# Kernel tuning notes

Hardware: AMD Instinct MI355X
Metric: run time of the kernel (lower is better)

The kernel has to match this reference:

```python
import jax, jax.numpy as jnp
import numpy as np

H = 12        # attention heads
WIN = 256     # one-sided sliding window (attention_window = 512)
L = 2         # encoder layers in this reference (full model: 12, same structure)
NEG = -1e9


def layer_norm(x, g, b, eps=1e-5):
    m = jnp.mean(x, axis=-1, keepdims=True)
    v = jnp.mean((x - m) ** 2, axis=-1, keepdims=True)
    return (x - m) * jax.lax.rsqrt(v + eps) * g + b


def heads(x):
    B, S, D = x.shape
    return x.reshape(B, S, H, D // H).transpose(0, 2, 1, 3)  # [B,H,S,Dh]


def overlap_chunks(x, w):
    # x: [B,H,S,D] -> [B,H,C,3w,D]; chunk c = keys/values seen by queries [c*w,(c+1)*w)
    B, Hh, S, D = x.shape
    xp = jnp.pad(x, ((0, 0), (0, 0), (w, w), (0, 0))).reshape(B, Hh, S // w + 2, w, D)
    return jnp.concatenate([xp[:, :, :-2], xp[:, :, 1:-1], xp[:, :, 2:]], axis=3)


def encoder_layer(x, mask, p):
    (Wq, bq, Wk, bk, Wv, bv, Wqg, bqg, Wkg, bkg, Wvg, bvg,
     Wo, bo, g1, b1n, W1, bf1, W2, bf2, g2, b2n) = p
    B, S, D = x.shape
    Dh = D // H
    w = WIN
    C = S // w
    scale = 1.0 / np.sqrt(Dh)
    q = heads(x @ Wq + bq)
    k = heads(x @ Wk + bk)
    v = heads(x @ Wv + bv)
    # --- sliding-window (banded) attention, chunked: each query chunk sees 3 key chunks ---
    qc = q.reshape(B, H, C, w, Dh)
    k3 = overlap_chunks(k, w)
    v3 = overlap_chunks(v, w)
    scores = jnp.einsum('bhcqd,bhckd->bhcqk', qc, k3) * scale  # [B,H,C,w,3w]
    qi = jnp.arange(w)[:, None]
    kr = jnp.arange(3 * w)[None, :] - w                       # key offset rel. to chunk start
    band = jnp.abs(kr - qi) <= w                              # [w,3w] |rel pos| <= w
    kpos = jnp.arange(C)[:, None] * w + (jnp.arange(3 * w) - w)[None, :]  # [C,3w] abs key idx
    inrange = (kpos >= 0) & (kpos < S)
    mp = jnp.pad(mask, ((0, 0), (w, w))).reshape(B, C + 2, w)
    m3 = jnp.concatenate([mp[:, :-2], mp[:, 1:-1], mp[:, 2:]], axis=2)  # [B,C,3w]
    loc_mask = band[None, :, :] & inrange[:, None, :]         # [C,w,3w]
    valid = loc_mask[None, None] & (m3 > 0)[:, None, :, None, :]
    scores = jnp.where(valid, scores, NEG)
    sloc = scores.reshape(B, H, S, 3 * w)
    # every token also attends to the global token (position 0)
    gsc = jnp.einsum('bhsd,bhd->bhs', q, k[:, :, 0]) * scale  # [B,H,S]
    attn = jax.nn.softmax(jnp.concatenate([sloc, gsc[..., None]], axis=-1), axis=-1)
    aloc = attn[..., :3 * w].reshape(B, H, C, w, 3 * w)
    ag = attn[..., -1]                                        # [B,H,S]
    out = jnp.einsum('bhcqk,bhckd->bhcqd', aloc, v3).reshape(B, H, S, Dh)
    out = out + ag[..., None] * v[:, :, 0][:, :, None, :]
    # --- global token full attention with separate global projections ---
    qg = heads(x @ Wqg + bqg)[:, :, 0]                        # [B,H,Dh]
    kg = heads(x @ Wkg + bkg)
    vg = heads(x @ Wvg + bvg)
    gs = jnp.where(mask[:, None, :] > 0,
                   jnp.einsum('bhd,bhsd->bhs', qg, kg) * scale, NEG)
    og = jnp.einsum('bhs,bhsd->bhd', jax.nn.softmax(gs, axis=-1), vg)
    out = out.at[:, :, 0].set(og)
    h = out.transpose(0, 2, 1, 3).reshape(B, S, D) @ Wo + bo
    x = layer_norm(x + h, g1, b1n)
    f = jax.nn.gelu(x @ W1 + bf1) @ W2 + bf2
    return layer_norm(x + f, g2, b2n)


def forward(input_ids, attention_mask, word_emb, pos_emb, ln_e_g, ln_e_b,
            Wq, bq, Wk, bk, Wv, bv, Wqg, bqg, Wkg, bkg, Wvg, bvg, Wo, bo,
            ln1_g, ln1_b, W1, bf1, W2, bf2, ln2_g, ln2_b, Wp, bp, Wc, bc):
    B, S = input_ids.shape
    x = word_emb[input_ids] + pos_emb[:S][None]
    x = layer_norm(x, ln_e_g, ln_e_b)
    for l in range(L):
        p = (Wq[l], bq[l], Wk[l], bk[l], Wv[l], bv[l], Wqg[l], bqg[l],
             Wkg[l], bkg[l], Wvg[l], bvg[l], Wo[l], bo[l], ln1_g[l], ln1_b[l],
             W1[l], bf1[l], W2[l], bf2[l], ln2_g[l], ln2_b[l])
        x = encoder_layer(x, attention_mask, p)
    pooled = jnp.tanh(x[:, 0] @ Wp + bp)   # BERT-style pooler on CLS
    return pooled @ Wc + bc


def setup_inputs() -> dict:
    B, S, D, V, F, NL = 2, 4096, 768, 50265, 3072, 2
    keys = iter(jax.random.split(jax.random.key(0), 64))
    def w(shape, s=0.02):
        return (jax.random.normal(next(keys), shape, jnp.float32) * s)
    inp = {
        'input_ids': jax.random.randint(next(keys), (B, S), 0, V),
        'attention_mask': jnp.ones((B, S), jnp.int32),
        'word_emb': w((V, D)), 'pos_emb': w((S, D)),
        'ln_e_g': jnp.ones((D,), jnp.float32), 'ln_e_b': jnp.zeros((D,), jnp.float32),
        'Wq': w((L, D, D)), 'bq': jnp.zeros((L, D), jnp.float32),
        'Wk': w((L, D, D)), 'bk': jnp.zeros((L, D), jnp.float32),
        'Wv': w((L, D, D)), 'bv': jnp.zeros((L, D), jnp.float32),
        'Wqg': w((L, D, D)), 'bqg': jnp.zeros((L, D), jnp.float32),
        'Wkg': w((L, D, D)), 'bkg': jnp.zeros((L, D), jnp.float32),
        'Wvg': w((L, D, D)), 'bvg': jnp.zeros((L, D), jnp.float32),
        'Wo': w((L, D, D)), 'bo': jnp.zeros((L, D), jnp.float32),
        'ln1_g': jnp.ones((L, D), jnp.float32), 'ln1_b': jnp.zeros((L, D), jnp.float32),
        'W1': w((L, D, F)), 'bf1': jnp.zeros((L, F), jnp.float32),
        'W2': w((L, F, D)), 'bf2': jnp.zeros((L, D), jnp.float32),
        'ln2_g': jnp.ones((L, D), jnp.float32), 'ln2_b': jnp.zeros((L, D), jnp.float32),
        'Wp': w((D, D)), 'bp': jnp.zeros((D,), jnp.float32),
        'Wc': w((D, NL)), 'bc': jnp.zeros((NL,), jnp.float32),
    }
    return inp


def reference(input_ids, attention_mask, word_emb, pos_emb, ln_e_g, ln_e_b,
              Wq, bq, Wk, bk, Wv, bv, Wqg, bqg, Wkg, bkg, Wvg, bvg, Wo, bo,
              ln1_g, ln1_b, W1, bf1, W2, bf2, ln2_g, ln2_b, Wp, bp, Wc, bc):
    return forward(input_ids, attention_mask, word_emb, pos_emb, ln_e_g, ln_e_b,
                   Wq, bq, Wk, bk, Wv, bv, Wqg, bqg, Wkg, bkg, Wvg, bvg, Wo, bo,
                   ln1_g, ln1_b, W1, bf1, W2, bf2, ln2_g, ln2_b, Wp, bp, Wc, bc)
```

## Files before the change

### kernel.cpp

```cpp
#include <hip/hip_runtime.h>
#include <hip/hip_bf16.h>
#include <math.h>

#define BB 2
#define SS 4096
#define DD 768
#define HH 12
#define DHH 64
#define WW 256
#define CC 16
#define FF 3072

typedef __attribute__((ext_vector_type(8))) short bf16x8;
typedef __attribute__((ext_vector_type(4))) float f32x4;

struct TP12 { const float* s[12]; unsigned short* d[12]; };
struct TP4  { const float* s[4];  unsigned short* d[4];  };

__device__ __forceinline__ float gelu_f(float x) {
    float u = 0.7978845608028654f * fmaf(0.044715f * x * x, x, x);
    return x / (1.f + __expf(-2.f * u));
}

__device__ __forceinline__ unsigned short bfb(float f) {
    __hip_bfloat16 h = __float2bfloat16(f);
    return *(unsigned short*)&h;
}

__device__ __forceinline__ float bf2f(unsigned short u) {
    return __uint_as_float(((unsigned int)u) << 16);
}

__device__ __forceinline__ void gload16(const void* g, void* l) {
    __builtin_amdgcn_global_load_lds(
        (const __attribute__((address_space(1))) unsigned int*)g,
        (__attribute__((address_space(3))) unsigned int*)l, 16, 0, 0);
}

__global__ __launch_bounds__(256) void transpose12_k(TP12 p)
{
    __shared__ float t[32][33];
    int z = blockIdx.z;
    const float* Wsrc = p.s[z];
    unsigned short* Wt = p.d[z];
    const int K = DD, N = DD;
    int n0 = blockIdx.x * 32, k0 = blockIdx.y * 32;
    int tx = threadIdx.x & 31, ty = threadIdx.x >> 5;
#pragma unroll
    for (int i = 0; i < 32; i += 8)
        t[ty + i][tx] = Wsrc[(size_t)(k0 + ty + i) * N + n0 + tx];
    __syncthreads();
#pragma unroll
    for (int i = 0; i < 32; i += 8)
        Wt[(size_t)(n0 + ty + i) * K + k0 + tx] = bfb(t[tx][ty + i]);
}

__global__ __launch_bounds__(256) void transposeR4_k(TP4 p)
{
    __shared__ float t[32][33];
    int z = blockIdx.z;
    const float* Wsrc = p.s[z];
    unsigned short* Wt = p.d[z];
    int K, N, n0, k0;
    if (z < 2) { K = DD; N = FF; n0 = blockIdx.x * 32; k0 = blockIdx.y * 32; }
    else { K = FF; N = DD; int cell = blockIdx.y * 96 + blockIdx.x;
           n0 = (cell % 24) * 32; k0 = (cell / 24) * 32; }
    int tx = threadIdx.x & 31, ty = threadIdx.x >> 5;
#pragma unroll
    for (int i = 0; i < 32; i += 8)
        t[ty + i][tx] = Wsrc[(size_t)(k0 + ty + i) * N + n0 + tx];
    __syncthreads();
#pragma unroll
    for (int i = 0; i < 32; i += 8)
        Wt[(size_t)(n0 + ty + i) * K + k0 + tx] = bfb(t[tx][ty + i]);
}

__global__ __launch_bounds__(256) void pack_bias5_k(const float* __restrict__ b0,
        const float* __restrict__ b1, const float* __restrict__ b2,
        const float* __restrict__ b3, const float* __restrict__ b4,
        float* __restrict__ dst)
{
    int gid = blockIdx.x * 256 + threadIdx.x;
    if (gid >= 2 * 5 * DD) return;
    int l = gid / (5 * DD), r = gid % (5 * DD), seg = r / DD, i = r % DD;
    const float* srcs[5] = { b0, b1, b2, b3, b4 };
    dst[gid] = srcs[seg][l * DD + i];
}

__global__ __launch_bounds__(256) void embed_ln_k(const int* __restrict__ ids,
        const float* __restrict__ wemb, const float* __restrict__ pemb,
        const float* __restrict__ g, const float* __restrict__ bta,
        float* __restrict__ x, unsigned short* __restrict__ xbf)
{
    int row = blockIdx.x;
    int s = row & (SS - 1);
    int tid = threadIdx.x;
    int lane = tid & 63, wvi = tid >> 6;
    __shared__ float red[8];
    float4 v = { 0.f, 0.f, 0.f, 0.f };
    if (tid < 192) {
        const float4* we = (const float4*)(wemb + (size_t)ids[row] * DD);
        const float4* pe = (const float4*)(pemb + (size_t)s * DD);
        float4 a = we[tid], b = pe[tid];
        v.x = a.x + b.x; v.y = a.y + b.y; v.z = a.z + b.z; v.w = a.w + b.w;
    }
    float sum = (v.x + v.y) + (v.z + v.w);
    float sq = fmaf(v.x, v.x, fmaf(v.y, v.y, fmaf(v.z, v.z, v.w * v.w)));
#pragma unroll
    for (int o = 1; o < 64; o <<= 1) {
        sum += __shfl_xor(sum, o);
        sq  += __shfl_xor(sq, o);
    }
    if (lane == 0) { red[wvi] = sum; red[4 + wvi] = sq; }
    __syncthreads();
    float S = (red[0] + red[1]) + (red[2] + red[3]);
    float Q = (red[4] + red[5]) + (red[6] + red[7]);
    float mean = S * (1.f / DD);
    float var = Q * (1.f / DD) - mean * mean;
    float rstd = rsqrtf(var + 1e-5f);
    if (tid < 192) {
        float4 gg = ((const float4*)g)[tid];
        float4 bb = ((const float4*)bta)[tid];
        float4 o;
        o.x = (v.x - mean) * rstd * gg.x + bb.x;
        o.y = (v.y - mean) * rstd * gg.y + bb.y;
        o.z = (v.z - mean) * rstd * gg.z + bb.z;
        o.w = (v.w - mean) * rstd * gg.w + bb.w;
        ((float4*)(x + (size_t)row * DD))[tid] = o;
        ushort4 ob = { bfb(o.x), bfb(o.y), bfb(o.z), bfb(o.w) };
        ((ushort4*)(xbf + (size_t)row * DD))[tid] = ob;
    }
}

__global__ __launch_bounds__(256) void add_ln_k(const float* __restrict__ xin,
        const float* __restrict__ hin, const float* __restrict__ g,
        const float* __restrict__ bta, float* __restrict__ xout,
        unsigned short* __restrict__ xbf)
{
    int row = blockIdx.x;
    int tid = threadIdx.x;
    int lane = tid & 63, wvi = tid >> 6;
    __shared__ float red[8];
    float4 v = { 0.f, 0.f, 0.f, 0.f };
    if (tid < 192) {
        float4 a = ((const float4*)(xin + (size_t)row * DD))[tid];
        float4 b = ((const float4*)(hin + (size_t)row * DD))[tid];
        v.x = a.x + b.x; v.y = a.y + b.y; v.z = a.z + b.z; v.w = a.w + b.w;
    }
    float sum = (v.x + v.y) + (v.z + v.w);
    float sq = fmaf(v.x, v.x, fmaf(v.y, v.y, fmaf(v.z, v.z, v.w * v.w)));
#pragma unroll
    for (int o = 1; o < 64; o <<= 1) {
        sum += __shfl_xor(sum, o);
        sq  += __shfl_xor(sq, o);
    }
    if (lane == 0) { red[wvi] = sum; red[4 + wvi] = sq; }
    __syncthreads();
    float S = (red[0] + red[1]) + (red[2] + red[3]);
    float Q = (red[4] + red[5]) + (red[6] + red[7]);
    float mean = S * (1.f / DD);
    float var = Q * (1.f / DD) - mean * mean;
    float rstd = rsqrtf(var + 1e-5f);
    if (tid < 192) {
        float4 gg = ((const float4*)g)[tid];
        float4 bb = ((const float4*)bta)[tid];
        float4 o;
        o.x = (v.x - mean) * rstd * gg.x + bb.x;
        o.y = (v.y - mean) * rstd * gg.y + bb.y;
        o.z = (v.z - mean) * rstd * gg.z + bb.z;
        o.w = (v.w - mean) * rstd * gg.w + bb.w;
        ((float4*)(xout + (size_t)row * DD))[tid] = o;
        ushort4 ob = { bfb(o.x), bfb(o.y), bfb(o.z), bfb(o.w) };
        ((ushort4*)(xbf + (size_t)row * DD))[tid] = ob;
    }
}

template<int OUT_BF16, int ACT_GELU>
__global__ __launch_bounds__(256) void mfma_gemm_k(
        const unsigned short* __restrict__ A,
        const unsigned short* __restrict__ Bt,
        const float* __restrict__ bias,
        void* __restrict__ Cv, int M, int N, int K)
{
    __shared__ short As[128 * 64];
    __shared__ short Bs[128 * 64];
    const int tid = threadIdx.x;
    const int lane = tid & 63, wv = tid >> 6;
    int nbx = gridDim.x;
    int nby = gridDim.y;
    int nwg = nbx * nby;
    int lid = blockIdx.y * nbx + blockIdx.x;
    int nid = ((nwg & 7) == 0) ? ((lid & 7) * (nwg >> 3) + (lid >> 3)) : lid;
    const int bm = (nid / nby) * 128, bn = (nid % nby) * 128;
    const int wm = wv >> 1, wn = wv & 1;

    const int srow0 = (tid * 16) >> 7;
    const int sbc   = (tid * 16) & 127;
    const int srcc  = sbc ^ ((srow0 & 7) << 4);
    const int ldst  = tid * 16;
    const char* Ab = (const char*)(A + (size_t)bm * K);
    const char* Bb = (const char*)(Bt + (size_t)bn * K);

    f32x4 acc[4][4];
#pragma unroll
    for (int i = 0; i < 4; i++)
#pragma unroll
        for (int j = 0; j < 4; j++) acc[i][j] = (f32x4){0.f, 0.f, 0.f, 0.f};

    const int lr = lane & 15;
    const int g = lane >> 4;
    const int rswz = (lr & 7) << 4;

    for (int k0 = 0; k0 < K; k0 += 64) {
        __syncthreads();
#pragma unroll
        for (int p = 0; p < 4; p++) {
            size_t roff = (size_t)(srow0 + p * 32) * (K * 2) + (size_t)k0 * 2 + srcc;
            gload16(Ab + roff, (char*)As + p * 4096 + ldst);
            gload16(Bb + roff, (char*)Bs + p * 4096 + ldst);
        }
        __syncthreads();
#pragma unroll
        for (int kk = 0; kk < 2; kk++) {
            int colb = (kk * 64 + g * 16) ^ rswz;
            bf16x8 af[4], bfr[4];
#pragma unroll
            for (int i = 0; i < 4; i++)
                af[i] = *(const bf16x8*)((const char*)As + (wm * 64 + i * 16 + lr) * 128 + colb);
#pragma unroll
            for (int j = 0; j < 4; j++)
                bfr[j] = *(const bf16x8*)((const char*)Bs + (wn * 64 + j * 16 + lr) * 128 + colb);
#pragma unroll
            for (int i = 0; i < 4; i++)
#pragma unroll
                for (int j = 0; j < 4; j++)
                    acc[i][j] = __builtin_amdgcn_mfma_f32_16x16x32_bf16(af[i], bfr[j], acc[i][j], 0, 0, 0);
        }
    }

    const int rq = lane >> 4;
#pragma unroll
    for (int j = 0; j < 4; j++) {
        int col = bn + wn * 64 + j * 16 + lr;
        float bv = bias[col];
#pragma unroll
        for (int i = 0; i < 4; i++) {
            int rowb = bm + wm * 64 + i * 16 + rq * 4;
#pragma unroll
            for (int r = 0; r < 4; r++) {
                float o = acc[i][j][r] + bv;
                if (ACT_GELU) o = gelu_f(o);
                if (OUT_BF16)
                    ((unsigned short*)Cv)[(size_t)(rowb + r) * N + col] = bfb(o);
                else
                    ((float*)Cv)[(size_t)(rowb + r) * N + col] = o;
            }
        }
    }
}

__global__ __launch_bounds__(256) void vtrans_k(const unsigned short* __restrict__ packed,
        unsigned short* __restrict__ vt)
{
    int s0 = blockIdx.x * 64, h = blockIdx.y, b = blockIdx.z;
    int tid = threadIdx.x;
    __shared__ unsigned short t[64][72];
    int r = tid >> 3, dc = (tid & 7) * 8;
#pragma unroll
    for (int half = 0; half < 2; half++) {
        int rr = r + half * 32;
        const unsigned short* src = packed + (size_t)(b * SS + s0 + rr) * 3840 + 2 * DD + h * 64 + dc;
        *(uint4*)&t[rr][dc] = *(const uint4*)src;
    }
    __syncthreads();
    int d = tid >> 3, sc = (tid & 7) * 8;
#pragma unroll
    for (int half = 0; half < 2; half++) {
        int dd2 = d + half * 32;
        unsigned short v[8];
#pragma unroll
        for (int e = 0; e < 8; e++) v[e] = t[sc + e][dd2];
        unsigned short* dst = vt + (size_t)((b * HH + h) * 64 + dd2) * SS + s0 + sc;
        *(uint4*)dst = *(uint4*)v;
    }
}

__global__ __launch_bounds__(256) void swin_mfma_k(
        const unsigned short* __restrict__ packed,
        const unsigned short* __restrict__ vt,
        const int* __restrict__ mask,
        unsigned short* __restrict__ O)
{
    __shared__ __align__(16) char smem[52736];
    const int c2 = blockIdx.x, h = blockIdx.y, b = blockIdx.z;
    const int tid = threadIdx.x;
    const int lane = tid & 63, wv = tid >> 6;
    const int l15 = lane & 15, g = lane >> 4;
    const int bh = b * HH + h;
    const int q0 = c2 * 128;

    char* PB = smem + 32768 + wv * 4096;
    float* maskAll = (float*)(smem + 49152);
    float* sA = (float*)(smem + 51712);
    float* sB = (float*)(smem + 52224);

    const char* pk_bytes = (const char*)packed;
    const char* vt_bytes = (const char*)vt;

    bf16x8 qf[2][2];
#pragma unroll
    for (int j = 0; j < 2; j++)
#pragma unroll
        for (int kk = 0; kk < 2; kk++)
            qf[j][kk] = *(const bf16x8*)(packed +
                (size_t)(b * SS + q0 + wv * 32 + j * 16 + l15) * 3840 + h * 64 + kk * 32 + g * 8);
    bf16x8 gkf[2];
#pragma unroll
    for (int kk = 0; kk < 2; kk++)
        gkf[kk] = *(const bf16x8*)(packed + (size_t)(b * SS) * 3840 + DD + h * 64 + kk * 32 + g * 8);
    float v0r[4];
#pragma unroll
    for (int jd = 0; jd < 4; jd++)
        v0r[jd] = bf2f(vt[(size_t)(bh * 64 + jd * 16 + l15) * SS]);

    f32x4 o_[2][4];
#pragma unroll
    for (int i = 0; i < 2; i++)
#pragma unroll
        for (int j = 0; j < 4; j++) o_[i][j] = (f32x4){0.f, 0.f, 0.f, 0.f};
    float m_[2] = { -1e20f, -1e20f };
    float l_[2] = { 0.f, 0.f };

    const int rswz = (l15 & 7) << 4;
    const int kt_s = max(0, 4 - 2 * c2);
    const int kt_e = min(10, 68 - 2 * c2);
    const int lo = wv >> 1;

    auto stage = [&](int ib, int kt) {
        const int kpos0 = q0 - 256 + kt * 64;
        char* KTd = smem + ib * 8192;
        char* VTd = smem + 16384 + ib * 8192;
        int off = tid * 16;
#pragma unroll
        for (int ch = 0; ch < 2; ch++) {
            int o2 = off + ch * 4096;
            int row = o2 >> 7, bc = o2 & 127;
            int srcc = bc ^ ((row & 7) << 4);
            gload16(pk_bytes + (size_t)(b * SS + kpos0 + row) * 7680 + 1536 + h * 128 + srcc,
                    KTd + o2);
            gload16(vt_bytes + (size_t)(bh * 64 + row) * 8192 + (size_t)(kpos0 * 2 + srcc),
                    VTd + o2);
        }
    };

    stage(0, kt_s);
    {
        int span = (kt_e - kt_s) * 64;
        int base_k = q0 - 256 + kt_s * 64;
        for (int idx = tid; idx < span; idx += 256) {
            int kp = base_k + idx;
            maskAll[kt_s * 64 + idx] = (mask[b * SS + kp] > 0) ? 0.f : -1e30f;
        }
    }
    __syncthreads();

    int cur = 0;
    for (int kt = kt_s; kt < kt_e; kt++) {
        if (kt + 1 < kt_e) stage(cur ^ 1, kt + 1);

        const int dl = kt - lo;
        if (dl >= 0 && dl <= 8) {
            const char* KT = smem + cur * 8192;
            const char* VT = smem + 16384 + cur * 8192;
            const bool edge = (dl == 0) || (dl == 8);

            f32x4 mrd[4];
#pragma unroll
            for (int i = 0; i < 4; i++)
                mrd[i] = *(const f32x4*)&maskAll[kt * 64 + i * 16 + g * 4];

            f32x4 s_[4][2];
#pragma unroll
            for (int i = 0; i < 4; i++)
#pragma unroll
                for (int j = 0; j < 2; j++) s_[i][j] = (f32x4){0.f, 0.f, 0.f, 0.f};
            __builtin_amdgcn_s_setprio(1);
#pragma unroll
            for (int kk = 0; kk < 2; kk++) {
                bf16x8 af[4];
#pragma unroll
                for (int i = 0; i < 4; i++)
                    af[i] = *(const bf16x8*)(KT + (i * 16 + l15) * 128 + ((kk * 64 + g * 16) ^ rswz));
#pragma unroll
                for (int i = 0; i < 4; i++)
#pragma unroll
                    for (int j = 0; j < 2; j++)
                        s_[i][j] = __builtin_amdgcn_mfma_f32_16x16x32_bf16(af[i], qf[j][kk], s_[i][j], 0, 0, 0);
            }
            __builtin_amdgcn_s_setprio(0);

#pragma unroll
            for (int j = 0; j < 2; j++) {
                float tm = -1e30f;
                if (edge) {
#pragma unroll
                    for (int i = 0; i < 4; i++) {
#pragma unroll
                        for (int r = 0; r < 4; r++) {
                            float v = fmaf(s_[i][j][r], 0.125f, mrd[i][r]);
                            int rel = kt * 64 - 256 + i * 16 + g * 4 + r - wv * 32 - j * 16 - l15;
                            v = (rel > 256 || rel < -256) ? -1e30f : v;
                            s_[i][j][r] = v;
                            tm = fmaxf(tm, v);
                        }
                    }
                } else {
#pragma unroll
                    for (int i = 0; i < 4; i++) {
#pragma unroll
                        for (int r = 0; r < 4; r++) {
                            float v = fmaf(s_[i][j][r], 0.125f, mrd[i][r]);
                            s_[i][j][r] = v;
                            tm = fmaxf(tm, v);
                        }
                    }
                }
                tm = fmaxf(tm, __shfl_xor(tm, 16));
                tm = fmaxf(tm, __shfl_xor(tm, 32));
                float mn = fmaxf(m_[j], tm);
                float fac = __expf(m_[j] - mn);
                m_[j] = mn;
                float ls = 0.f;
                int q32 = j * 16 + l15;
#pragma unroll
                for (int i = 0; i < 4; i++) {
                    float p0 = __expf(s_[i][j][0] - mn);
                    float p1 = __expf(s_[i][j][1] - mn);
                    float p2 = __expf(s_[i][j][2] - mn);
                    float p3 = __expf(s_[i][j][3] - mn);
                    ls += (p0 + p1) + (p2 + p3);
                    uint2 pw;
                    pw.x = (unsigned int)bfb(p0) | ((unsigned int)bfb(p1) << 16);
                    pw.y = (unsigned int)bfb(p2) | ((unsigned int)bfb(p3) << 16);
                    *(uint2*)(PB + q32 * 128 + ((i * 32 + g * 8) ^ rswz)) = pw;
                }
                ls += __shfl_xor(ls, 16);
                ls += __shfl_xor(ls, 32);
                l_[j] = l_[j] * fac + ls;
                if (g == 0) sA[wv * 32 + q32] = fac;
            }

#pragma unroll
            for (int iq = 0; iq < 2; iq++) {
                f32x4 fc = *(const f32x4*)&sA[wv * 32 + iq * 16 + g * 4];
#pragma unroll
                for (int jd = 0; jd < 4; jd++)
#pragma unroll
                    for (int r = 0; r < 4; r++) o_[iq][jd][r] *= fc[r];
            }
            __builtin_amdgcn_s_setprio(1);
#pragma unroll
            for (int kk = 0; kk < 2; kk++) {
                bf16x8 pa[2], vb[4];
#pragma unroll
                for (int iq = 0; iq < 2; iq++)
                    pa[iq] = *(const bf16x8*)(PB + (iq * 16 + l15) * 128 + ((kk * 64 + g * 16) ^ rswz));
#pragma unroll
                for (int jd = 0; jd < 4; jd++)
                    vb[jd] = *(const bf16x8*)(VT + (jd * 16 + l15) * 128 + ((kk * 64 + g * 16) ^ rswz));
#pragma unroll
                for (int iq = 0; iq < 2; iq++)
#pragma unroll
                    for (int jd = 0; jd < 4; jd++)
                        o_[iq][jd] = __builtin_amdgcn_mfma_f32_16x16x32_bf16(pa[iq], vb[jd], o_[iq][jd], 0, 0, 0);
            }
            __builtin_amdgcn_s_setprio(0);
        }

        asm volatile("s_waitcnt vmcnt(0)" ::: "memory");
        __builtin_amdgcn_sched_barrier(0);
        __builtin_amdgcn_s_barrier();
        __builtin_amdgcn_sched_barrier(0);
        cur ^= 1;
    }

#pragma unroll
    for (int j = 0; j < 2; j++) {
        float pd = 0.f;
#pragma unroll
        for (int kk = 0; kk < 2; kk++)
#pragma unroll
            for (int e = 0; e < 8; e++)
                pd += bf2f((unsigned short)qf[j][kk][e]) * bf2f((unsigned short)gkf[kk][e]);
        pd += __shfl_xor(pd, 16);
        pd += __shfl_xor(pd, 32);
        float sg = pd * 0.125f;
        float mf = fmaxf(m_[j], sg);
        float fac = __expf(m_[j] - mf);
        float pg = __expf(sg - mf);
        float lf = l_[j] * fac + pg;
        float inv = 1.f / lf;
        if (g == 0) {
            sA[wv * 32 + j * 16 + l15] = fac * inv;
            sB[wv * 32 + j * 16 + l15] = pg * inv;
        }
    }
#pragma unroll
    for (int iq = 0; iq < 2; iq++) {
        f32x4 fA = *(const f32x4*)&sA[wv * 32 + iq * 16 + g * 4];
        f32x4 fB = *(const f32x4*)&sB[wv * 32 + iq * 16 + g * 4];
#pragma unroll
        for (int jd = 0; jd < 4; jd++) {
#pragma unroll
            for (int r = 0; r < 4; r++) {
                float val = o_[iq][jd][r] * fA[r] + fB[r] * v0r[jd];
                int row = b * SS + q0 + wv * 32 + iq * 16 + g * 4 + r;
                O[(size_t)row * DD + h * 64 + jd * 16 + l15] = bfb(val);
            }
        }
    }
}

__global__ __launch_bounds__(256) void gattn1_k(const float* __restrict__ qg,
        const unsigned short* __restrict__ packed, const int* __restrict__ mask,
        float* __restrict__ pm, float* __restrict__ pl, float* __restrict__ po)
{
    int cc = blockIdx.x, h = blockIdx.y, b = blockIdx.z;
    int tid = threadIdx.x;
    __shared__ float qs[64], red[256], ps[256], ored[4][64];
    if (tid < 64) qs[tid] = qg[b * DD + h * 64 + tid];
    __syncthreads();
    int s = cc * 256 + tid;
    const unsigned short* kr = packed + (size_t)(b * SS + s) * 3840 + 3 * DD + h * 64;
    float a = 0.f;
#pragma unroll
    for (int d8 = 0; d8 < 8; d8++) {
        bf16x8 kv = *(const bf16x8*)(kr + d8 * 8);
#pragma unroll
        for (int e = 0; e < 8; e++)
            a = fmaf(qs[d8 * 8 + e], bf2f((unsigned short)kv[e]), a);
    }
    a *= 0.125f;
    float sv = (mask[b * SS + s] > 0) ? a : -1e9f;
    red[tid] = sv; __syncthreads();
    for (int o = 128; o > 0; o >>= 1) {
        if (tid < o) red[tid] = fmaxf(red[tid], red[tid + o]);
        __syncthreads();
    }
    float mx = red[0]; __syncthreads();
    float p = __expf(sv - mx);
    ps[tid] = p;
    red[tid] = p; __syncthreads();
    for (int o = 128; o > 0; o >>= 1) {
        if (tid < o) red[tid] += red[tid + o];
        __syncthreads();
    }
    float ls = red[0];
    int d = tid & 63, grp = tid >> 6;
    const unsigned short* vgb = packed + 4 * DD + h * 64 + d;
    float oa = 0.f;
    for (int t = 0; t < 64; t++) {
        int srow = cc * 256 + grp * 64 + t;
        oa = fmaf(ps[grp * 64 + t], bf2f(vgb[(size_t)(b * SS + srow) * 3840]), oa);
    }
    ored[grp][d] = oa; __syncthreads();
    if (tid < 64) {
        int idx = (b * HH + h) * 16 + cc;
        po[(size_t)idx * 64 + tid] = ored[0][tid] + ored[1][tid] + ored[2][tid] + ored[3][tid];
        if (tid == 0) { pm[idx] = mx; pl[idx] = ls; }
    }
}

__global__ __launch_bounds__(64) void gattn2_k(const float* __restrict__ pm,
        const float* __restrict__ pl, const float* __restrict__ po,
        unsigned short* __restrict__ O)
{
    int h = blockIdx.x, b = blockIdx.y;
    int tid = threadIdx.x;
    int base = (b * HH + h) * 16;
    float mx = -1e30f;
    for (int c2 = 0; c2 < 16; c2++) mx = fmaxf(mx, pm[base + c2]);
    float den = 0.f, oa = 0.f;
    for (int c2 = 0; c2 < 16; c2++) {
        float w = __expf(pm[base + c2] - mx);
        den = fmaf(pl[base + c2], w, den);
        oa = fmaf(po[(size_t)(base + c2) * 64 + tid], w, oa);
    }
    O[(size_t)(b * SS) * DD + h * 64 + tid] = bfb(oa / den);
}

template<int ACT_TANH>
__global__ __launch_bounds__(256) void rowgemv_k(const float* __restrict__ x,
        size_t xstride, const float* __restrict__ W, const float* __restrict__ bias,
        float* __restrict__ dst, int N)
{
    int b = blockIdx.y;
    int colL = threadIdx.x & 63, part = threadIdx.x >> 6;
    int col = blockIdx.x * 64 + colL;
    __shared__ float partial[4][64];
    const float* xr = x + (size_t)b * xstride;
    float a = 0.f;
    for (int k = part * (DD / 4); k < (part + 1) * (DD / 4); k++)
        a = fmaf(xr[k], W[(size_t)k * N + col], a);
    partial[part][colL] = a; __syncthreads();
    if (part == 0) {
        float s = partial[0][colL] + partial[1][colL] + partial[2][colL] + partial[3][colL]
                + bias[col];
        if (ACT_TANH) s = tanhf(s);
        dst[b * N + col] = s;
    }
}

__global__ __launch_bounds__(256) void cls_k(const float* __restrict__ pooled,
        const float* __restrict__ Wc, const float* __restrict__ bc,
        float* __restrict__ out)
{
    int lane = threadIdx.x & 63, pair = threadIdx.x >> 6;
    int b = pair >> 1, cls = pair & 1;
    float a = 0.f;
#pragma unroll
    for (int j = 0; j < 12; j++) {
        int k = lane + j * 64;
        a = fmaf(pooled[b * DD + k], Wc[k * 2 + cls], a);
    }
#pragma unroll
    for (int o = 1; o < 64; o <<= 1) a += __shfl_xor(a, o);
    if (lane == 0) out[b * 2 + cls] = a + bc[cls];
}

extern "C" void kernel_launch(void* const* d_in, const int* in_sizes, int n_in,
                              void* d_out, int out_size, void* d_ws, size_t ws_size,
                              hipStream_t stream) {
    const int*   input_ids = (const int*)d_in[0];
    const int*   amask     = (const int*)d_in[1];
    const float* word_emb  = (const float*)d_in[2];
    const float* pos_emb   = (const float*)d_in[3];
    const float* ln_e_g    = (const float*)d_in[4];
    const float* ln_e_b    = (const float*)d_in[5];
    const float* Wq  = (const float*)d_in[6];  const float* bq  = (const float*)d_in[7];
    const float* Wk  = (const float*)d_in[8];  const float* bk  = (const float*)d_in[9];
    const float* Wv  = (const float*)d_in[10]; const float* bv  = (const float*)d_in[11];
    const float* Wqg = (const float*)d_in[12]; const float* bqg = (const float*)d_in[13];
    const float* Wkg = (const float*)d_in[14]; const float* bkg = (const float*)d_in[15];
    const float* Wvg = (const float*)d_in[16]; const float* bvg = (const float*)d_in[17];
    const float* Wo  = (const float*)d_in[18]; const float* bo  = (const float*)d_in[19];
    const float* ln1_g = (const float*)d_in[20]; const float* ln1_b = (const float*)d_in[21];
    const float* W1  = (const float*)d_in[22]; const float* bf1 = (const float*)d_in[23];
    const float* W2  = (const float*)d_in[24]; const float* bf2 = (const float*)d_in[25];
    const float* ln2_g = (const float*)d_in[26]; const float* ln2_b = (const float*)d_in[27];
    const float* Wp  = (const float*)d_in[28]; const float* bp  = (const float*)d_in[29];
    const float* Wc  = (const float*)d_in[30]; const float* bc  = (const float*)d_in[31];
    float* out = (float*)d_out;

    char* wsb = (char*)d_ws;
    float*          x      = (float*)(wsb + 0);
    unsigned short* xbf    = (unsigned short*)(wsb + 25165824);
    unsigned short* packed = (unsigned short*)(wsb + 37748736);
    unsigned short* vtb    = (unsigned short*)(wsb + 100663296);
    unsigned short* aout   = (unsigned short*)(wsb + 113246208);
    float*          hf     = (float*)(wsb + 125829120);
    char*           wts    = wsb + 150994944;
    float*          b5     = (float*)(wsb + 184025088);
    float*          qg     = (float*)(wsb + 184055808);
    float*          pm     = (float*)(wsb + 184061952);
    float*          pl     = (float*)(wsb + 184063488);
    float*          po     = (float*)(wsb + 184065024);
    float*          pooled = (float*)(wsb + 184163328);
    unsigned short* mid    = packed;

    const size_t SQ = (size_t)DD * DD;
    const size_t PER_L = (6 * SQ + 2 * (size_t)DD * FF) * 2;
    unsigned short* Wt5[2], *Wo_t[2], *W1_t[2], *W2_t[2];
    for (int l = 0; l < 2; l++) {
        char* base = wts + (size_t)l * PER_L;
        Wt5[l]  = (unsigned short*)base;
        Wo_t[l] = (unsigned short*)(base + 5 * SQ * 2);
        W1_t[l] = (unsigned short*)(base + 6 * SQ * 2);
        W2_t[l] = (unsigned short*)(base + 6 * SQ * 2 + (size_t)DD * FF * 2);
    }

    const int M = BB * SS;

    TP12 t12;
    for (int l = 0; l < 2; l++) {
        t12.s[l * 6 + 0] = Wq  + (size_t)l * SQ;  t12.d[l * 6 + 0] = Wt5[l] + 0 * SQ;
        t12.s[l * 6 + 1] = Wk  + (size_t)l * SQ;  t12.d[l * 6 + 1] = Wt5[l] + 1 * SQ;
        t12.s[l * 6 + 2] = Wv  + (size_t)l * SQ;  t12.d[l * 6 + 2] = Wt5[l] + 2 * SQ;
        t12.s[l * 6 + 3] = Wkg + (size_t)l * SQ;  t12.d[l * 6 + 3] = Wt5[l] + 3 * SQ;
        t12.s[l * 6 + 4] = Wvg + (size_t)l * SQ;  t12.d[l * 6 + 4] = Wt5[l] + 4 * SQ;
        t12.s[l * 6 + 5] = Wo  + (size_t)l * SQ;  t12.d[l * 6 + 5] = Wo_t[l];
    }
    TP4 t4;
    t4.s[0] = W1;                      t4.d[0] = W1_t[0];
    t4.s[1] = W1 + (size_t)DD * FF;    t4.d[1] = W1_t[1];
    t4.s[2] = W2;                      t4.d[2] = W2_t[0];
    t4.s[3] = W2 + (size_t)FF * DD;    t4.d[3] = W2_t[1];

    transpose12_k<<<dim3(24, 24, 12), 256, 0, stream>>>(t12);
    transposeR4_k<<<dim3(96, 24, 4), 256, 0, stream>>>(t4);
    pack_bias5_k<<<(2 * 5 * DD + 255) / 256, 256, 0, stream>>>(bq, bk, bv, bkg, bvg, b5);

    embed_ln_k<<<M, 256, 0, stream>>>(input_ids, word_emb, pos_emb, ln_e_g, ln_e_b, x, xbf);

    dim3 gqkv(M / 128, 3840 / 128);
    dim3 g768(M / 128, DD / 128);
    dim3 g3072(M / 128, FF / 128);

    for (int l = 0; l < 2; l++) {
        const float* Wqg_l = Wqg + (size_t)l * SQ; const float* bqg_l = bqg + (size_t)l * DD;
        const float* bo_l  = bo  + (size_t)l * DD;
        const float* bf1_l = bf1 + (size_t)l * FF;
        const float* bf2_l = bf2 + (size_t)l * DD;
        const float* g1_l  = ln1_g + (size_t)l * DD; const float* b1_l = ln1_b + (size_t)l * DD;
        const float* g2_l  = ln2_g + (size_t)l * DD; const float* b2_l = ln2_b + (size_t)l * DD;

        mfma_gemm_k<1, 0><<<gqkv, 256, 0, stream>>>(xbf, Wt5[l], b5 + (size_t)l * 3840,
                                                    packed, M, 3840, DD);
        vtrans_k<<<dim3(SS / 64, HH, BB), 256, 0, stream>>>(packed, vtb);
        rowgemv_k<0><<<dim3(DD / 64, BB), 256, 0, stream>>>(x, (size_t)SS * DD, Wqg_l, bqg_l, qg, DD);

        swin_mfma_k<<<dim3(SS / 128, HH, BB), 256, 0, stream>>>(packed, vtb, amask, aout);
        gattn1_k<<<dim3(16, HH, BB), 256, 0, stream>>>(qg, packed, amask, pm, pl, po);
        gattn2_k<<<dim3(HH, BB), 64, 0, stream>>>(pm, pl, po, aout);

        mfma_gemm_k<0, 0><<<g768, 256, 0, stream>>>(aout, Wo_t[l], bo_l, hf, M, DD, DD);
        add_ln_k<<<M, 256, 0, stream>>>(x, hf, g1_l, b1_l, x, xbf);

        mfma_gemm_k<1, 1><<<g3072, 256, 0, stream>>>(xbf, W1_t[l], bf1_l, mid, M, FF, DD);
        mfma_gemm_k<0, 0><<<g768, 256, 0, stream>>>(mid, W2_t[l], bf2_l, hf, M, DD, FF);
        add_ln_k<<<M, 256, 0, stream>>>(x, hf, g2_l, b2_l, x, xbf);
    }

    rowgemv_k<1><<<dim3(DD / 64, BB), 256, 0, stream>>>(x, (size_t)SS * DD, Wp, bp, pooled, DD);
    cls_k<<<1, 256, 0, stream>>>(pooled, Wc, bc, out);
}
```

Baseline: 711.5 us.

## Double-buffer LDS tiles in MFMA GEMM to overlap global loads with compute

The bf16 MFMA GEMM now keeps two 128x64 LDS buffers for A and B and issues the next k-tile's direct-to-LDS loads before computing on the current tile. Each iteration uses a single vmcnt wait plus barrier instead of two __syncthreads around a blocking load. This is meant to hide global memory latency behind the MFMA work. In exchange LDS use doubles to 64KB per block, which may lower occupancy.

```diff
diff --git a/kernel.cpp b/kernel.cpp
--- a/kernel.cpp
+++ b/kernel.cpp
@@ -182,8 +182,8 @@
         const float* __restrict__ bias,
         void* __restrict__ Cv, int M, int N, int K)
 {
-    __shared__ short As[128 * 64];
-    __shared__ short Bs[128 * 64];
+    __shared__ short As[2 * 128 * 64];
+    __shared__ short Bs[2 * 128 * 64];
     const int tid = threadIdx.x;
     const int lane = tid & 63, wv = tid >> 6;
     int nbx = gridDim.x;
@@ -210,32 +210,50 @@
     const int lr = lane & 15;
     const int g = lane >> 4;
     const int rswz = (lr & 7) << 4;
-
-    for (int k0 = 0; k0 < K; k0 += 64) {
-        __syncthreads();
+    const int NK = K >> 6;
+
+    auto stage = [&](int ib, int t) {
+        const int k0 = t << 6;
+        char* Ad = (char*)As + ib * 16384;
+        char* Bd = (char*)Bs + ib * 16384;
 #pragma unroll
         for (int p = 0; p < 4; p++) {
             size_t roff = (size_t)(srow0 + p * 32) * (K * 2) + (size_t)k0 * 2 + srcc;
-            gload16(Ab + roff, (char*)As + p * 4096 + ldst);
-            gload16(Bb + roff, (char*)Bs + p * 4096 + ldst);
+            gload16(Ab + roff, Ad + p * 4096 + ldst);
+            gload16(Bb + roff, Bd + p * 4096 + ldst);
         }
-        __syncthreads();
+    };
+
+    stage(0, 0);
+    asm volatile("s_waitcnt vmcnt(0)" ::: "memory");
+    __builtin_amdgcn_s_barrier();
+
+    int cur = 0;
+    for (int t = 0; t < NK; t++) {
+        if (t + 1 < NK) stage(cur ^ 1, t + 1);
+        const char* Ar = (const char*)As + cur * 16384;
+        const char* Br = (const char*)Bs + cur * 16384;
 #pragma unroll
         for (int kk = 0; kk < 2; kk++) {
             int colb = (kk * 64 + g * 16) ^ rswz;
             bf16x8 af[4], bfr[4];
 #pragma unroll
             for (int i = 0; i < 4; i++)
-                af[i] = *(const bf16x8*)((const char*)As + (wm * 64 + i * 16 + lr) * 128 + colb);
+                af[i] = *(const bf16x8*)(Ar + (wm * 64 + i * 16 + lr) * 128 + colb);
 #pragma unroll
             for (int j = 0; j < 4; j++)
-                bfr[j] = *(const bf16x8*)((const char*)Bs + (wn * 64 + j * 16 + lr) * 128 + colb);
+                bfr[j] = *(const bf16x8*)(Br + (wn * 64 + j * 16 + lr) * 128 + colb);
 #pragma unroll
             for (int i = 0; i < 4; i++)
 #pragma unroll
                 for (int j = 0; j < 4; j++)
                     acc[i][j] = __builtin_amdgcn_mfma_f32_16x16x32_bf16(af[i], bfr[j], acc[i][j], 0, 0, 0);
         }
+        asm volatile("s_waitcnt vmcnt(0)" ::: "memory");
+        __builtin_amdgcn_sched_barrier(0);
+        __builtin_amdgcn_s_barrier();
+        __builtin_amdgcn_sched_barrier(0);
+        cur ^= 1;
     }
 
     const int rq = lane >> 4;
```

After: 686.3 us. 3.5% less time.
